# Optimization experiments

Measured on AMD Instinct MI355X. Metric: run time of the kernel, lower is better.

## Reference

```python
import jax, jax.numpy as jnp
import numpy as np

N_OPCODES = 31
B, S, D = 64, 16, 1024
MAX_STEPS = 16


def setup_inputs() -> dict:
    key = jax.random.key(0)
    k1, k2, k3, k4 = jax.random.split(key, 4)
    return {
        "opcode_logits": jax.random.normal(k1, (B, S, N_OPCODES), dtype=jnp.float32),
        "operands": jax.random.normal(k2, (B, S, 4), dtype=jnp.float32),
        "signal": jax.random.normal(k3, (B, D), dtype=jnp.float32),
        "op_kernels": jax.random.normal(k4, (N_OPCODES, D, D), dtype=jnp.float32) * 0.01,
    }


def reference(opcode_logits, operands, signal, op_kernels):
    # opcode_logits: (B,S,O), operands: (B,S,4), signal: (B,D), op_kernels: (O,D,D)
    n_steps = min(opcode_logits.shape[1], MAX_STEPS)
    weights = jax.nn.softmax(opcode_logits, axis=-1)  # (B,S,O)

    # time-major inputs for scan: (n_steps, B, O) and (n_steps, B, 1)
    ws = jnp.swapaxes(weights[:, :n_steps], 0, 1)
    gate_logits = jnp.swapaxes(operands[:, :n_steps, 3:4], 0, 1)

    def step(h, inputs):
        w, gl = inputs  # (B,O), (B,1)
        gate = jax.nn.sigmoid(gl)
        # equivalent to h @ (sum_o w_o K_o) but never forms the (B,D,D) kernel
        transformed = jnp.einsum('bo,bd,odk->bk', w, h, op_kernels)
        h_new = gate * transformed + (1.0 - gate) * h
        return h_new, None

    h, _ = jax.lax.scan(step, signal, (ws, gate_logits))
    return h
```

## Files before the change

### kernel.cpp

```cpp
#include <hip/hip_runtime.h>
#include <cstddef>
#include <cstdint>

#define NB 64
#define ND 1024
#define NO 31
#define NSTEPS 16
#define KS 62
#define KT32 992
#define KC32 16

typedef _Float16 half8 __attribute__((ext_vector_type(8)));
typedef float floatx4 __attribute__((ext_vector_type(4)));

__global__ void softmax_k(const float* __restrict__ logits, float* __restrict__ W) {
    int row = blockIdx.x * blockDim.x + threadIdx.x;
    if (row >= NB * NSTEPS) return;
    const float* x = logits + (size_t)row * NO;
    float m = -1e30f;
    for (int o = 0; o < NO; ++o) m = fmaxf(m, x[o]);
    float e[NO]; float s = 0.f;
    for (int o = 0; o < NO; ++o) { e[o] = expf(x[o] - m); s += e[o]; }
    float inv = 1.0f / s;
    float* wo = W + (size_t)row * NO;
    for (int o = 0; o < NO; ++o) wo[o] = e[o] * inv;
}

__global__ __launch_bounds__(256) void kconv_k(const float* __restrict__ K,
                                               _Float16* __restrict__ Ktf) {
    __shared__ float tile[32 * 256];
    int kt  = blockIdx.x >> 2;
    int nb4 = blockIdx.x & 3;
    int tid = threadIdx.x;
    int lane = tid & 63, w = tid >> 6;

    {
        const float* src = K + ((size_t)kt * 32) * ND + nb4 * 256;
        #pragma unroll
        for (int i = 0; i < 8; ++i) {
            int r = i * 4 + w;
            int x = lane * 4;
            int xs = x ^ (((r >> 3) & 1) << 4);
            float4 v = *(const float4*)(src + (size_t)r * ND + x);
            *(float4*)&tile[r * 256 + xs] = v;
        }
    }
    __syncthreads();

    int kl0 = (lane >> 4) * 8;
    int swz = ((lane >> 4) & 1) << 4;
    #pragma unroll
    for (int i = 0; i < 4; ++i) {
        int ns_local = i * 4 + w;
        int nl = ns_local * 16 + (lane & 15);
        int xsw = nl ^ swz;
        half8 v;
        #pragma unroll
        for (int j = 0; j < 8; ++j) v[j] = (_Float16)tile[(kl0 + j) * 256 + xsw];
        int ns = nb4 * 16 + ns_local;
        size_t unit = ((size_t)ns * KT32 + kt) * 64 + lane;
        *(half8*)(Ktf + unit * 8) = v;
    }
}

__global__ __launch_bounds__(256) void gemm_k(
    const float* __restrict__ h, const _Float16* __restrict__ Ktf,
    const float* __restrict__ W, float* __restrict__ P, int step)
{
    __shared__ _Float16 lds_a[64 * 512];
    int nb = blockIdx.x;
    int ks = blockIdx.y;
    int tid = threadIdx.x;
    int l = tid & 63, w = tid >> 6;
    int o = ks >> 1;
    int d_base = (ks & 1) * 512;
    int ml = l & 15, q = l >> 4;
    int ns0 = nb * 16 + w * 4;

    const half8* bp0 = (const half8*)Ktf + ((size_t)(ns0 + 0) * KT32 + (size_t)ks * KC32) * 64 + l;
    const half8* bp1 = (const half8*)Ktf + ((size_t)(ns0 + 1) * KT32 + (size_t)ks * KC32) * 64 + l;
    const half8* bp2 = (const half8*)Ktf + ((size_t)(ns0 + 2) * KT32 + (size_t)ks * KC32) * 64 + l;
    const half8* bp3 = (const half8*)Ktf + ((size_t)(ns0 + 3) * KT32 + (size_t)ks * KC32) * 64 + l;
    half8 bc0 = bp0[0], bc1 = bp1[0], bc2 = bp2[0], bc3 = bp3[0];

    {
        int sb = tid >> 2, su = tid & 3;
        float wv = W[((size_t)sb * NSTEPS + step) * NO + o];
        const float* hb = h + (size_t)sb * ND + d_base;
        #pragma unroll
        for (int li = 0; li < 16; ++li) {
            int p = li * 4 + su;
            float4 x0 = *(const float4*)(hb + p * 8);
            float4 x1 = *(const float4*)(hb + p * 8 + 4);
            half8 v;
            v[0] = (_Float16)(x0.x * wv); v[1] = (_Float16)(x0.y * wv);
            v[2] = (_Float16)(x0.z * wv); v[3] = (_Float16)(x0.w * wv);
            v[4] = (_Float16)(x1.x * wv); v[5] = (_Float16)(x1.y * wv);
            v[6] = (_Float16)(x1.z * wv); v[7] = (_Float16)(x1.w * wv);
            *(half8*)&lds_a[(size_t)(p * 64 + sb) * 8] = v;
        }
    }
    __syncthreads();

    const half8* Ap = (const half8*)lds_a;
    floatx4 acc[4][4] = {};
    #pragma unroll
    for (int s = 0; s < KC32; ++s) {
        half8 bn0, bn1, bn2, bn3;
        if (s < KC32 - 1) {
            bn0 = bp0[(size_t)(s + 1) * 64];
            bn1 = bp1[(size_t)(s + 1) * 64];
            bn2 = bp2[(size_t)(s + 1) * 64];
            bn3 = bp3[(size_t)(s + 1) * 64];
        }
        int abase = (s * 4 + q) * 64 + ml;
        half8 a0 = Ap[abase];
        half8 a1 = Ap[abase + 16];
        half8 a2 = Ap[abase + 32];
        half8 a3 = Ap[abase + 48];
        acc[0][0] = __builtin_amdgcn_mfma_f32_16x16x32_f16(a0, bc0, acc[0][0], 0, 0, 0);
        acc[0][1] = __builtin_amdgcn_mfma_f32_16x16x32_f16(a1, bc0, acc[0][1], 0, 0, 0);
        acc[0][2] = __builtin_amdgcn_mfma_f32_16x16x32_f16(a2, bc0, acc[0][2], 0, 0, 0);
        acc[0][3] = __builtin_amdgcn_mfma_f32_16x16x32_f16(a3, bc0, acc[0][3], 0, 0, 0);
        acc[1][0] = __builtin_amdgcn_mfma_f32_16x16x32_f16(a0, bc1, acc[1][0], 0, 0, 0);
        acc[1][1] = __builtin_amdgcn_mfma_f32_16x16x32_f16(a1, bc1, acc[1][1], 0, 0, 0);
        acc[1][2] = __builtin_amdgcn_mfma_f32_16x16x32_f16(a2, bc1, acc[1][2], 0, 0, 0);
        acc[1][3] = __builtin_amdgcn_mfma_f32_16x16x32_f16(a3, bc1, acc[1][3], 0, 0, 0);
        acc[2][0] = __builtin_amdgcn_mfma_f32_16x16x32_f16(a0, bc2, acc[2][0], 0, 0, 0);
        acc[2][1] = __builtin_amdgcn_mfma_f32_16x16x32_f16(a1, bc2, acc[2][1], 0, 0, 0);
        acc[2][2] = __builtin_amdgcn_mfma_f32_16x16x32_f16(a2, bc2, acc[2][2], 0, 0, 0);
        acc[2][3] = __builtin_amdgcn_mfma_f32_16x16x32_f16(a3, bc2, acc[2][3], 0, 0, 0);
        acc[3][0] = __builtin_amdgcn_mfma_f32_16x16x32_f16(a0, bc3, acc[3][0], 0, 0, 0);
        acc[3][1] = __builtin_amdgcn_mfma_f32_16x16x32_f16(a1, bc3, acc[3][1], 0, 0, 0);
        acc[3][2] = __builtin_amdgcn_mfma_f32_16x16x32_f16(a2, bc3, acc[3][2], 0, 0, 0);
        acc[3][3] = __builtin_amdgcn_mfma_f32_16x16x32_f16(a3, bc3, acc[3][3], 0, 0, 0);
        if (s < KC32 - 1) { bc0 = bn0; bc1 = bn1; bc2 = bn2; bc3 = bn3; }
    }

    float* Pks = P + (size_t)ks * (NB * ND);
    #pragma unroll
    for (int t = 0; t < 4; ++t) {
        int n = (ns0 + t) * 16 + ml;
        #pragma unroll
        for (int mt = 0; mt < 4; ++mt) {
            #pragma unroll
            for (int r = 0; r < 4; ++r) {
                int b = mt * 16 + q * 4 + r;
                Pks[(size_t)b * ND + n] = acc[t][mt][r];
            }
        }
    }
}

__global__ void update_k(const float* __restrict__ hin, const float* __restrict__ P,
                         const float* __restrict__ operands, float* __restrict__ hout,
                         int step)
{
    __shared__ float red[256];
    int tid = threadIdx.x;
    int w = tid >> 6, lane = tid & 63;
    int j = (w & 1) * 64 + lane;
    int g = blockIdx.x * 128 + j;
    const float* p = P + (size_t)((w >> 1) * 31) * (NB * ND) + g;
    float s = 0.f;
    #pragma unroll
    for (int i = 0; i < 31; ++i) s += p[(size_t)i * (NB * ND)];
    red[(w >> 1) * 128 + j] = s;
    __syncthreads();
    if (tid < 128) {
        float tot = red[tid] + red[tid + 128];
        int g2 = blockIdx.x * 128 + tid;
        int b = g2 >> 10;
        float gl = operands[((size_t)b * NSTEPS + step) * 4 + 3];
        float gt = 1.0f / (1.0f + expf(-gl));
        hout[g2] = gt * tot + (1.0f - gt) * hin[g2];
    }
}

extern "C" void kernel_launch(void* const* d_in, const int* in_sizes, int n_in,
                              void* d_out, int out_size, void* d_ws, size_t ws_size,
                              hipStream_t stream)
{
    const float* logits   = (const float*)d_in[0];
    const float* operands = (const float*)d_in[1];
    const float* signal   = (const float*)d_in[2];
    const float* opk      = (const float*)d_in[3];
    float* out = (float*)d_out;
    char* ws = (char*)d_ws;

    size_t offW = 0;
    size_t offP = 131072;
    size_t offH = offP + (size_t)KS * NB * ND * 4;
    size_t offK = offH + 2ull * NB * ND * 4;

    float*    W  = (float*)(ws + offW);
    float*    P  = (float*)(ws + offP);
    float*    h0 = (float*)(ws + offH);
    float*    h1 = h0 + NB * ND;
    _Float16* Ktf = (_Float16*)(ws + offK);

    softmax_k<<<dim3(4), 256, 0, stream>>>(logits, W);
    kconv_k<<<dim3(3968), 256, 0, stream>>>(opk, Ktf);

    const float* hc = signal;
    float* hn = h0;
    for (int t = 0; t < NSTEPS; ++t) {
        gemm_k<<<dim3(4, KS), 256, 0, stream>>>(hc, Ktf, W, P, t);
        float* dst = (t == NSTEPS - 1) ? out : hn;
        update_k<<<dim3(512), 256, 0, stream>>>(hc, P, operands, dst, t);
        hc = dst;
        hn = (hn == h0) ? h1 : h0;
    }
}
```

Measured before the change: 532.6 us.

## Drop split-K partials: one block per opcode over full K, narrower N tile

```diff
diff --git a/kernel.cpp b/kernel.cpp
--- a/kernel.cpp
+++ b/kernel.cpp
@@ -6,9 +6,8 @@
 #define ND 1024
 #define NO 31
 #define NSTEPS 16
-#define KS 62
+#define KS 31
 #define KT32 992
-#define KC32 16
 
 typedef _Float16 half8 __attribute__((ext_vector_type(8)));
 typedef float floatx4 __attribute__((ext_vector_type(4)));
@@ -69,84 +68,77 @@
 {
     __shared__ _Float16 lds_a[64 * 512];
     int nb = blockIdx.x;
-    int ks = blockIdx.y;
+    int o  = blockIdx.y;
     int tid = threadIdx.x;
     int l = tid & 63, w = tid >> 6;
-    int o = ks >> 1;
-    int d_base = (ks & 1) * 512;
     int ml = l & 15, q = l >> 4;
-    int ns0 = nb * 16 + w * 4;
-
-    const half8* bp0 = (const half8*)Ktf + ((size_t)(ns0 + 0) * KT32 + (size_t)ks * KC32) * 64 + l;
-    const half8* bp1 = (const half8*)Ktf + ((size_t)(ns0 + 1) * KT32 + (size_t)ks * KC32) * 64 + l;
-    const half8* bp2 = (const half8*)Ktf + ((size_t)(ns0 + 2) * KT32 + (size_t)ks * KC32) * 64 + l;
-    const half8* bp3 = (const half8*)Ktf + ((size_t)(ns0 + 3) * KT32 + (size_t)ks * KC32) * 64 + l;
-    half8 bc0 = bp0[0], bc1 = bp1[0], bc2 = bp2[0], bc3 = bp3[0];
-
-    {
-        int sb = tid >> 2, su = tid & 3;
-        float wv = W[((size_t)sb * NSTEPS + step) * NO + o];
-        const float* hb = h + (size_t)sb * ND + d_base;
-        #pragma unroll
-        for (int li = 0; li < 16; ++li) {
-            int p = li * 4 + su;
-            float4 x0 = *(const float4*)(hb + p * 8);
-            float4 x1 = *(const float4*)(hb + p * 8 + 4);
-            half8 v;
-            v[0] = (_Float16)(x0.x * wv); v[1] = (_Float16)(x0.y * wv);
-            v[2] = (_Float16)(x0.z * wv); v[3] = (_Float16)(x0.w * wv);
-            v[4] = (_Float16)(x1.x * wv); v[5] = (_Float16)(x1.y * wv);
-            v[6] = (_Float16)(x1.z * wv); v[7] = (_Float16)(x1.w * wv);
-            *(half8*)&lds_a[(size_t)(p * 64 + sb) * 8] = v;
-        }
-    }
-    __syncthreads();
-
-    const half8* Ap = (const half8*)lds_a;
-    floatx4 acc[4][4] = {};
+    int ns0 = nb * 8 + w * 2;
+    int sb = tid >> 2, su = tid & 3;
+
+    const half8* bp0 = (const half8*)Ktf + ((size_t)(ns0 + 0) * KT32 + (size_t)o * 32) * 64 + l;
+    const half8* bp1 = (const half8*)Ktf + ((size_t)(ns0 + 1) * KT32 + (size_t)o * 32) * 64 + l;
+
+    half8 bc0 = bp0[0], bc1 = bp1[0];
+
+    floatx4 acc[2][4] = {};
+    float wv = W[((size_t)sb * NSTEPS + step) * NO + o];
+
     #pragma unroll
-    for (int s = 0; s < KC32; ++s) {
-        half8 bn0, bn1, bn2, bn3;
-        if (s < KC32 - 1) {
-            bn0 = bp0[(size_t)(s + 1) * 64];
-            bn1 = bp1[(size_t)(s + 1) * 64];
-            bn2 = bp2[(size_t)(s + 1) * 64];
-            bn3 = bp3[(size_t)(s + 1) * 64];
-        }
-        int abase = (s * 4 + q) * 64 + ml;
-        half8 a0 = Ap[abase];
-        half8 a1 = Ap[abase + 16];
-        half8 a2 = Ap[abase + 32];
-        half8 a3 = Ap[abase + 48];
-        acc[0][0] = __builtin_amdgcn_mfma_f32_16x16x32_f16(a0, bc0, acc[0][0], 0, 0, 0);
-        acc[0][1] = __builtin_amdgcn_mfma_f32_16x16x32_f16(a1, bc0, acc[0][1], 0, 0, 0);
-        acc[0][2] = __builtin_amdgcn_mfma_f32_16x16x32_f16(a2, bc0, acc[0][2], 0, 0, 0);
-        acc[0][3] = __builtin_amdgcn_mfma_f32_16x16x32_f16(a3, bc0, acc[0][3], 0, 0, 0);
-        acc[1][0] = __builtin_amdgcn_mfma_f32_16x16x32_f16(a0, bc1, acc[1][0], 0, 0, 0);
-        acc[1][1] = __builtin_amdgcn_mfma_f32_16x16x32_f16(a1, bc1, acc[1][1], 0, 0, 0);
-        acc[1][2] = __builtin_amdgcn_mfma_f32_16x16x32_f16(a2, bc1, acc[1][2], 0, 0, 0);
-        acc[1][3] = __builtin_amdgcn_mfma_f32_16x16x32_f16(a3, bc1, acc[1][3], 0, 0, 0);
-        acc[2][0] = __builtin_amdgcn_mfma_f32_16x16x32_f16(a0, bc2, acc[2][0], 0, 0, 0);
-        acc[2][1] = __builtin_amdgcn_mfma_f32_16x16x32_f16(a1, bc2, acc[2][1], 0, 0, 0);
-        acc[2][2] = __builtin_amdgcn_mfma_f32_16x16x32_f16(a2, bc2, acc[2][2], 0, 0, 0);
-        acc[2][3] = __builtin_amdgcn_mfma_f32_16x16x32_f16(a3, bc2, acc[2][3], 0, 0, 0);
-        acc[3][0] = __builtin_amdgcn_mfma_f32_16x16x32_f16(a0, bc3, acc[3][0], 0, 0, 0);
-        acc[3][1] = __builtin_amdgcn_mfma_f32_16x16x32_f16(a1, bc3, acc[3][1], 0, 0, 0);
-        acc[3][2] = __builtin_amdgcn_mfma_f32_16x16x32_f16(a2, bc3, acc[3][2], 0, 0, 0);
-        acc[3][3] = __builtin_amdgcn_mfma_f32_16x16x32_f16(a3, bc3, acc[3][3], 0, 0, 0);
-        if (s < KC32 - 1) { bc0 = bn0; bc1 = bn1; bc2 = bn2; bc3 = bn3; }
-    }
-
-    float* Pks = P + (size_t)ks * (NB * ND);
+    for (int p2 = 0; p2 < 2; ++p2) {
+        if (p2) __syncthreads();
+        {
+            const float* hb = h + (size_t)sb * ND + p2 * 512;
+            #pragma unroll
+            for (int li = 0; li < 16; ++li) {
+                int p = li * 4 + su;
+                float4 x0 = *(const float4*)(hb + p * 8);
+                float4 x1 = *(const float4*)(hb + p * 8 + 4);
+                half8 v;
+                v[0] = (_Float16)(x0.x * wv); v[1] = (_Float16)(x0.y * wv);
+                v[2] = (_Float16)(x0.z * wv); v[3] = (_Float16)(x0.w * wv);
+                v[4] = (_Float16)(x1.x * wv); v[5] = (_Float16)(x1.y * wv);
+                v[6] = (_Float16)(x1.z * wv); v[7] = (_Float16)(x1.w * wv);
+                *(half8*)&lds_a[(size_t)(p * 64 + sb) * 8] = v;
+            }
+        }
+        __syncthreads();
+
+        const half8* Ap = (const half8*)lds_a;
+        #pragma unroll
+        for (int s = 0; s < 16; ++s) {
+            int gs = p2 * 16 + s;
+            half8 bn0, bn1;
+            if (gs < 31) {
+                bn0 = bp0[(size_t)(gs + 1) * 64];
+                bn1 = bp1[(size_t)(gs + 1) * 64];
+            }
+            int abase = (s * 4 + q) * 64 + ml;
+            half8 a0 = Ap[abase];
+            half8 a1 = Ap[abase + 16];
+            half8 a2 = Ap[abase + 32];
+            half8 a3 = Ap[abase + 48];
+            acc[0][0] = __builtin_amdgcn_mfma_f32_16x16x32_f16(a0, bc0, acc[0][0], 0, 0, 0);
+            acc[0][1] = __builtin_amdgcn_mfma_f32_16x16x32_f16(a1, bc0, acc[0][1], 0, 0, 0);
+            acc[0][2] = __builtin_amdgcn_mfma_f32_16x16x32_f16(a2, bc0, acc[0][2], 0, 0, 0);
+            acc[0][3] = __builtin_amdgcn_mfma_f32_16x16x32_f16(a3, bc0, acc[0][3], 0, 0, 0);
+            acc[1][0] = __builtin_amdgcn_mfma_f32_16x16x32_f16(a0, bc1, acc[1][0], 0, 0, 0);
+            acc[1][1] = __builtin_amdgcn_mfma_f32_16x16x32_f16(a1, bc1, acc[1][1], 0, 0, 0);
+            acc[1][2] = __builtin_amdgcn_mfma_f32_16x16x32_f16(a2, bc1, acc[1][2], 0, 0, 0);
+            acc[1][3] = __builtin_amdgcn_mfma_f32_16x16x32_f16(a3, bc1, acc[1][3], 0, 0, 0);
+            if (gs < 31) { bc0 = bn0; bc1 = bn1; }
+        }
+    }
+
+    float* Po = P + (size_t)o * (NB * ND);
     #pragma unroll
-    for (int t = 0; t < 4; ++t) {
+    for (int t = 0; t < 2; ++t) {
         int n = (ns0 + t) * 16 + ml;
         #pragma unroll
         for (int mt = 0; mt < 4; ++mt) {
             #pragma unroll
             for (int r = 0; r < 4; ++r) {
                 int b = mt * 16 + q * 4 + r;
-                Pks[(size_t)b * ND + n] = acc[t][mt][r];
+                Po[(size_t)b * ND + n] = acc[t][mt][r];
             }
         }
     }
@@ -159,13 +151,19 @@
     __shared__ float red[256];
     int tid = threadIdx.x;
     int w = tid >> 6, lane = tid & 63;
+    int half = w >> 1;
     int j = (w & 1) * 64 + lane;
     int g = blockIdx.x * 128 + j;
-    const float* p = P + (size_t)((w >> 1) * 31) * (NB * ND) + g;
+    const float* p = P + (size_t)(half * 16) * (NB * ND) + g;
     float s = 0.f;
-    #pragma unroll
-    for (int i = 0; i < 31; ++i) s += p[(size_t)i * (NB * ND)];
-    red[(w >> 1) * 128 + j] = s;
+    if (half == 0) {
+        #pragma unroll
+        for (int i = 0; i < 16; ++i) s += p[(size_t)i * (NB * ND)];
+    } else {
+        #pragma unroll
+        for (int i = 0; i < 15; ++i) s += p[(size_t)i * (NB * ND)];
+    }
+    red[half * 128 + j] = s;
     __syncthreads();
     if (tid < 128) {
         float tot = red[tid] + red[tid + 128];
@@ -205,7 +203,7 @@
     const float* hc = signal;
     float* hn = h0;
     for (int t = 0; t < NSTEPS; ++t) {
-        gemm_k<<<dim3(4, KS), 256, 0, stream>>>(hc, Ktf, W, P, t);
+        gemm_k<<<dim3(8, KS), 256, 0, stream>>>(hc, Ktf, W, P, t);
         float* dst = (t == NSTEPS - 1) ? out : hn;
         update_k<<<dim3(512), 256, 0, stream>>>(hc, P, operands, dst, t);
         hc = dst;
```

New measurement: 539.9 us. No clear change (+1.4%).
